# Kernel tuning notes

Measured on AMD Instinct MI355X. Metric: run time of the kernel, lower is better.

The kernel has to match this reference:

```python
import jax, jax.numpy as jnp
import numpy as np

C = 512
NUM_HEADS = 8
RF = 4          # reduction_factor
GROUPS = 8      # min(8, C//8)
EPS = 1e-5


def _pos_enc(h, w, c):
    # matches torch _create_positional_encoding; c must be divisible by 4
    y = jnp.arange(h, dtype=jnp.float32)[:, None] * jnp.ones((1, w), jnp.float32)
    x = jnp.ones((h, 1), jnp.float32) * jnp.arange(w, dtype=jnp.float32)[None, :]
    div = jnp.exp(jnp.arange(0, c // 2, 2, dtype=jnp.float32) * (-np.log(10000.0) / (c // 2)))  # [c//4]
    d = div[:, None, None]
    sy, cy = jnp.sin(y[None] * d), jnp.cos(y[None] * d)   # [c//4,h,w]
    sx, cx = jnp.sin(x[None] * d), jnp.cos(x[None] * d)
    pe = jnp.stack([sy, cy, sx, cx], axis=1).reshape(c, h, w)  # interleaved 0::4..3::4
    return pe[None] * 0.01


def _group_norm(x, w, b):
    B, Cc, H, W = x.shape
    g = x.reshape(B, GROUPS, -1)
    m = g.mean(-1, keepdims=True)
    v = g.var(-1, keepdims=True)
    g = (g - m) / jnp.sqrt(v + EPS)
    return g.reshape(B, Cc, H, W) * w[None, :, None, None] + b[None, :, None, None]


def setup_inputs() -> dict:
    key = jax.random.key(0)
    ks = jax.random.split(key, 4)
    B, H, W = 1, 256, 256
    x = jax.random.normal(ks[0], (B, C, H, W), jnp.float32)
    qkv_w = jax.random.normal(ks[1], (3 * C, C), jnp.float32) * 0.02
    proj_w = jax.random.normal(ks[2], (C, C), jnp.float32) * 0.02
    gamma = jax.random.normal(ks[3], (1,), jnp.float32)
    return {
        "x": x,
        "gn_weight": jnp.ones((C,), jnp.float32),
        "gn_bias": jnp.zeros((C,), jnp.float32),
        "qkv_w": qkv_w,
        "proj_w": proj_w,
        "proj_b": jnp.zeros((C,), jnp.float32),
        "gamma": gamma,
        "temperature": jnp.ones((NUM_HEADS, 1, 1), jnp.float32),
    }


def reference(x, gn_weight, gn_bias, qkv_w, proj_w, proj_b, gamma, temperature):
    B, Cc, H, W = x.shape
    hd = Cc // NUM_HEADS
    identity = x
    xn = _group_norm(x, gn_weight, gn_bias)
    # spatial reduction (AvgPool2d k=4 s=4); H,W > 32 in this config
    Hr, Wr = H // RF, W // RF
    xr = xn.reshape(B, Cc, Hr, RF, Wr, RF).mean(axis=(3, 5))
    xr = xr + _pos_enc(Hr, Wr, Cc)
    qkv = jnp.einsum('oc,bchw->bohw', qkv_w, xr)  # 1x1 conv, no bias
    q, k, v = jnp.split(qkv, 3, axis=1)
    N = Hr * Wr
    q = q.reshape(B, NUM_HEADS, hd, N) * (hd ** -0.5) * temperature[None]
    k = k.reshape(B, NUM_HEADS, hd, N)
    v = v.reshape(B, NUM_HEADS, hd, N)
    # chunked attention in torch == plain softmax attention (chunking over queries)
    attn = jax.nn.softmax(jnp.einsum('bhdn,bhdm->bhnm', q, k), axis=-1)
    out = jnp.einsum('bhnm,bhdm->bhdn', attn, v).reshape(B, Cc, Hr, Wr)
    out = jax.image.resize(out, (B, Cc, H, W), method='bilinear')  # align_corners=False
    out = jnp.einsum('oc,bchw->bohw', proj_w, out) + proj_b[None, :, None, None]
    # dropout in eval mode is identity
    return identity + gamma * out
```

## Files before the change

### kernel.cpp

```cpp
#include <hip/hip_runtime.h>
#include <hip/hip_bf16.h>


typedef __attribute__((ext_vector_type(4))) short short4v;
typedef __attribute__((ext_vector_type(8))) short short8v;
typedef __attribute__((ext_vector_type(4))) float f32x4;
typedef __attribute__((ext_vector_type(4))) unsigned int u32x4;

#define MFMA16(a, b, c) __builtin_amdgcn_mfma_f32_16x16x32_bf16(a, b, c, 0, 0, 0)

__device__ __forceinline__ unsigned short bf16r(float f) {
    unsigned int u = __builtin_bit_cast(unsigned int, f);
    u += 0x7fffu + ((u >> 16) & 1u);
    return (unsigned short)(u >> 16);
}
__device__ __forceinline__ float bff(unsigned short s) {
    unsigned int u = ((unsigned int)s) << 16;
    return __builtin_bit_cast(float, u);
}
__device__ __forceinline__ unsigned int fbits(float f) {
    return __builtin_bit_cast(unsigned int, f);
}

__global__ __launch_bounds__(256) void k_wconv(const float* __restrict__ qkv_w,
                                               const float* __restrict__ proj_w,
                                               const float* __restrict__ temp,
                                               unsigned short* __restrict__ wq_b,
                                               unsigned short* __restrict__ wp_b) {
    int idx = blockIdx.x * 256 + threadIdx.x;
    const int NQ = 1536 * 512;
    if (idx < NQ) {
        int o = idx >> 9;
        float sc = (o < 512) ? temp[o >> 6] * 0.125f : 1.0f;
        wq_b[idx] = bf16r(qkv_w[idx] * sc);
    } else {
        int j = idx - NQ;
        wp_b[j] = bf16r(proj_w[j]);
    }
}

__global__ __launch_bounds__(256) void k_pool(const float* __restrict__ x,
                                              float* __restrict__ xp,
                                              float* __restrict__ partials) {
    int hr = blockIdx.x;
    int c  = blockIdx.y;
    int t = threadIdx.x;
    int r = t >> 6, wq = t & 63;
    const float4* src = (const float4*)(x + (size_t)c * 65536 + (size_t)(4 * hr + r) * 256 + 4 * wq);
    float4 v = *src;
    float s4 = v.x + v.y + v.z + v.w;
    float q4 = v.x * v.x + v.y * v.y + v.z * v.z + v.w * v.w;

    __shared__ float sm[256];
    __shared__ float wq4[4];
    sm[t] = s4;
    float qq = q4;
#pragma unroll
    for (int off = 1; off < 64; off <<= 1) qq += __shfl_xor(qq, off, 64);
    if ((t & 63) == 0) wq4[t >> 6] = qq;
    __syncthreads();
    if (t < 64) {
        float cs = sm[t] + sm[64 + t] + sm[128 + t] + sm[192 + t];
        xp[(size_t)c * 4096 + hr * 64 + t] = cs * (1.0f / 16.0f);
        float ts = cs;
#pragma unroll
        for (int off = 1; off < 64; off <<= 1) ts += __shfl_xor(ts, off, 64);
        if (t == 0) {
            int g = c >> 6;
            int slot = (c & 63) * 64 + hr;
            partials[(size_t)(g * 4096 + slot) * 2 + 0] = ts;
            partials[(size_t)(g * 4096 + slot) * 2 + 1] = wq4[0] + wq4[1] + wq4[2] + wq4[3];
        }
    }
}

__global__ __launch_bounds__(256) void k_stats(const float* __restrict__ partials,
                                               float* __restrict__ gstats) {
    int g = blockIdx.x;
    int t = threadIdx.x;
    float s = 0.f, q = 0.f;
    for (int i = t; i < 4096; i += 256) {
        s += partials[(size_t)(g * 4096 + i) * 2 + 0];
        q += partials[(size_t)(g * 4096 + i) * 2 + 1];
    }
#pragma unroll
    for (int off = 1; off < 64; off <<= 1) {
        s += __shfl_xor(s, off, 64);
        q += __shfl_xor(q, off, 64);
    }
    __shared__ float ss[4], qs[4];
    if ((t & 63) == 0) { ss[t >> 6] = s; qs[t >> 6] = q; }
    __syncthreads();
    if (t == 0) {
        float S = ss[0] + ss[1] + ss[2] + ss[3];
        float Q = qs[0] + qs[1] + qs[2] + qs[3];
        const float inv = 1.0f / 4194304.0f;
        float m = S * inv;
        float var = Q * inv - m * m;
        gstats[2 * g] = m;
        gstats[2 * g + 1] = rsqrtf(var + 1e-5f);
    }
}

__global__ __launch_bounds__(256) void k_xr(const float* __restrict__ xp,
                                            const float* __restrict__ gs,
                                            const float* __restrict__ gw,
                                            const float* __restrict__ gb,
                                            unsigned short* __restrict__ xr) {
    int idx = blockIdx.x * 256 + threadIdx.x;
    int c = idx >> 12, n = idx & 4095;
    int hr = n >> 6, wr = n & 63;
    int g = c >> 6;
    float m = gs[2 * g], rs = gs[2 * g + 1];
    float xn = (xp[idx] - m) * rs * gw[c] + gb[c];
    int i = c >> 2, kind = c & 3;
    float di = expf(-(float)i * 0.07195578415606394f);
    float arg = ((kind < 2) ? (float)hr : (float)wr) * di;
    float pe = 0.01f * ((kind & 1) ? cosf(arg) : sinf(arg));
    xr[idx] = bf16r(xn + pe);
}

__global__ __launch_bounds__(256) void k_gemm(const unsigned short* __restrict__ A,
                                              const unsigned short* __restrict__ B,
                                              unsigned short* __restrict__ C) {
    __shared__ unsigned short As[128][36];
    __shared__ unsigned short Bs[128][36];
    int t = threadIdx.x;
    int w = t >> 6, l = t & 63, l15 = l & 15, lg = l >> 4;
    int wrow = w >> 1, wcol = w & 1;
    int m0 = blockIdx.y * 128, n0 = blockIdx.x * 128;
    f32x4 acc[4][4] = {};

    for (int k0 = 0; k0 < 512; k0 += 32) {
#pragma unroll
        for (int i = 0; i < 4; i++) {
            int idx = t + 256 * i;
            int row = idx >> 3, kc = idx & 7;
            short4v av = *(const short4v*)(A + (size_t)(m0 + row) * 512 + k0 + 4 * kc);
            *(short4v*)&As[row][4 * kc] = av;
        }
#pragma unroll
        for (int i = 0; i < 4; i++) {
            int idx = t + 256 * i;
            int kr = idx >> 5, nc = idx & 31;
            short4v bv = *(const short4v*)(B + (size_t)(k0 + kr) * 4096 + n0 + 4 * nc);
#pragma unroll
            for (int j = 0; j < 4; j++) Bs[4 * nc + j][kr] = (unsigned short)bv[j];
        }
        __syncthreads();

        short8v af[4];
#pragma unroll
        for (int mi = 0; mi < 4; mi++) {
            int ar = wrow * 64 + mi * 16 + l15;
            short4v a0 = *(const short4v*)&As[ar][4 * lg];
            short4v a1 = *(const short4v*)&As[ar][16 + 4 * lg];
            af[mi] = __builtin_shufflevector(a0, a1, 0, 1, 2, 3, 4, 5, 6, 7);
        }
#pragma unroll
        for (int ni = 0; ni < 4; ni++) {
            int bc = wcol * 64 + ni * 16 + l15;
            short4v b0 = *(const short4v*)&Bs[bc][4 * lg];
            short4v b1 = *(const short4v*)&Bs[bc][16 + 4 * lg];
            short8v bf = __builtin_shufflevector(b0, b1, 0, 1, 2, 3, 4, 5, 6, 7);
#pragma unroll
            for (int mi = 0; mi < 4; mi++) acc[mi][ni] = MFMA16(af[mi], bf, acc[mi][ni]);
        }
        __syncthreads();
    }
#pragma unroll
    for (int mi = 0; mi < 4; mi++)
#pragma unroll
        for (int ni = 0; ni < 4; ni++) {
            int row = m0 + wrow * 64 + mi * 16 + 4 * lg;
            int col = n0 + wcol * 64 + ni * 16 + l15;
#pragma unroll
            for (int r = 0; r < 4; r++)
                C[(size_t)(row + r) * 4096 + col] = bf16r(acc[mi][ni][r]);
        }
}

__global__ __launch_bounds__(256) void k_perm(const unsigned short* __restrict__ qkv,
                                              unsigned short* __restrict__ qtg,
                                              unsigned short* __restrict__ ktg,
                                              unsigned short* __restrict__ vtg) {
    __shared__ unsigned short lt[64][40];
    int t = threadIdx.x;
    int tile = blockIdx.x, h = blockIdx.y, z = blockIdx.z;
    int base = (z == 0 ? 0 : (z == 1 ? 512 : 1024)) + h * 64;
    int r = t >> 2, c4 = (t & 3) * 8;
    *(short8v*)&lt[r][c4] = *(const short8v*)(qkv + (size_t)(base + r) * 4096 + tile * 32 + c4);
    __syncthreads();
    unsigned short o[8];
    if (z < 2) {
        int col = t & 31, lgc = (t >> 5) & 3, s = t >> 7;
#pragma unroll
        for (int j = 0; j < 4; j++) {
            o[j] = lt[s * 32 + 4 * lgc + j][col];
            o[4 + j] = lt[s * 32 + 16 + 4 * lgc + j][col];
        }
    } else {
        int d = t & 63, lgc = t >> 6;
#pragma unroll
        for (int j = 0; j < 4; j++) {
            o[j] = lt[d][4 * lgc + j];
            o[4 + j] = lt[d][16 + 4 * lgc + j];
        }
    }
    unsigned short* dst = (z == 0 ? qtg : (z == 1 ? ktg : vtg)) + ((size_t)h * 128 + tile) * 2048 + t * 8;
    *(short8v*)dst = *(const short8v*)o;
}

__global__ __launch_bounds__(128) void k_attn(const unsigned short* __restrict__ qtg,
                                              const unsigned short* __restrict__ ktg,
                                              const unsigned short* __restrict__ vtg,
                                              unsigned short* __restrict__ opart,
                                              float* __restrict__ mlg) {
    int t = threadIdx.x;
    int l = t & 63, l15 = l & 15, lg = l >> 4, mw = t >> 6;
    int nu = blockIdx.x * 2 + mw, h = blockIdx.y, seg = blockIdx.z;

    const unsigned short* qb = qtg + ((size_t)h * 128 + nu) * 2048;
    const unsigned short* kb = ktg + ((size_t)h * 128 + seg * 32) * 2048;
    const unsigned short* vb = vtg + ((size_t)h * 128 + seg * 32) * 2048;

    short8v qf[2][2];
#pragma unroll
    for (int ng = 0; ng < 2; ng++)
#pragma unroll
        for (int s = 0; s < 2; s++)
            qf[ng][s] = *(const short8v*)(qb + s * 1024 + lg * 256 + ng * 128 + l15 * 8);

    f32x4 od[2][4] = {};
    float mrun[2] = {0.f, 0.f};
    float lrun[2] = {0.f, 0.f};
    const float LOG2E = 1.44269504f;

    auto loadK = [&](short8v (&kf)[2][2], int kt) {
#pragma unroll
        for (int mf = 0; mf < 2; mf++)
#pragma unroll
            for (int s = 0; s < 2; s++)
                kf[mf][s] = *(const short8v*)(kb + kt * 2048 + s * 1024 + lg * 256 + mf * 128 + l15 * 8);
    };
    auto loadV = [&](short8v (&vf)[4], int kt) {
#pragma unroll
        for (int dg = 0; dg < 4; dg++)
            vf[dg] = *(const short8v*)(vb + kt * 2048 + lg * 512 + dg * 128 + l15 * 8);
    };
    auto compute = [&](const short8v (&kf)[2][2], const short8v (&vf)[4]) {
#pragma unroll
        for (int ng = 0; ng < 2; ng++) {
            f32x4 s0 = {}, s1 = {};
            __builtin_amdgcn_s_setprio(1);
            s0 = MFMA16(kf[0][0], qf[ng][0], s0);
            s0 = MFMA16(kf[0][1], qf[ng][1], s0);
            s1 = MFMA16(kf[1][0], qf[ng][0], s1);
            s1 = MFMA16(kf[1][1], qf[ng][1], s1);
            __builtin_amdgcn_s_setprio(0);
            float pm = fmaxf(fmaxf(fmaxf(s0[0], s0[1]), fmaxf(s0[2], s0[3])),
                             fmaxf(fmaxf(s1[0], s1[1]), fmaxf(s1[2], s1[3])));
            pm = fmaxf(pm, __shfl_xor(pm, 16, 64));
            pm = fmaxf(pm, __shfl_xor(pm, 32, 64));
            if (!__all(pm <= mrun[ng] + 8.f)) {
                float mnew = fmaxf(mrun[ng], pm);
                float alpha = __expf(mrun[ng] - mnew);
#pragma unroll
                for (int dg = 0; dg < 4; dg++)
#pragma unroll
                    for (int r = 0; r < 4; r++) od[ng][dg][r] *= alpha;
                lrun[ng] *= alpha;
                mrun[ng] = mnew;
            }
            float mc = mrun[ng] * LOG2E;
            float p0[4], p1[4];
            float ps = 0.f;
#pragma unroll
            for (int r = 0; r < 4; r++) {
                p0[r] = __builtin_amdgcn_exp2f(fmaf(s0[r], LOG2E, -mc));
                p1[r] = __builtin_amdgcn_exp2f(fmaf(s1[r], LOG2E, -mc));
                ps += p0[r] + p1[r];
            }
            ps += __shfl_xor(ps, 16, 64);
            ps += __shfl_xor(ps, 32, 64);
            lrun[ng] += ps;
            u32x4 P;
            P[0] = __builtin_amdgcn_perm(fbits(p0[1]), fbits(p0[0]), 0x07060302u);
            P[1] = __builtin_amdgcn_perm(fbits(p0[3]), fbits(p0[2]), 0x07060302u);
            P[2] = __builtin_amdgcn_perm(fbits(p1[1]), fbits(p1[0]), 0x07060302u);
            P[3] = __builtin_amdgcn_perm(fbits(p1[3]), fbits(p1[2]), 0x07060302u);
            short8v pb = __builtin_bit_cast(short8v, P);
            __builtin_amdgcn_s_setprio(1);
#pragma unroll
            for (int dg = 0; dg < 4; dg++) od[ng][dg] = MFMA16(vf[dg], pb, od[ng][dg]);
            __builtin_amdgcn_s_setprio(0);
        }
    };

    short8v kfA[2][2], kfB[2][2], vfA[4], vfB[4];
    loadK(kfA, 0);
#pragma unroll 1
    for (int kt = 0; kt < 32; kt += 2) {
        loadV(vfA, kt);
        loadK(kfB, kt + 1);
        compute(kfA, vfA);
        loadV(vfB, kt + 1);
        if (kt + 2 < 32) loadK(kfA, kt + 2);
        compute(kfB, vfB);
    }

    unsigned short* op = opart + ((size_t)(seg * 512 + h * 64)) * 4096 + nu * 32;
#pragma unroll
    for (int ng = 0; ng < 2; ng++)
#pragma unroll
        for (int dg = 0; dg < 4; dg++)
#pragma unroll
            for (int r = 0; r < 4; r++) {
                int d = dg * 16 + 4 * lg + r;
                op[(size_t)d * 4096 + ng * 16 + l15] = bf16r(od[ng][dg][r]);
            }
    if (lg == 0) {
#pragma unroll
        for (int ng = 0; ng < 2; ng++) {
            float* mo = mlg + ((size_t)(seg * 8 + h) * 4096 + nu * 32 + ng * 16 + l15) * 2;
            mo[0] = mrun[ng];
            mo[1] = lrun[ng];
        }
    }
}

__global__ __launch_bounds__(256) void k_merge(const unsigned short* __restrict__ opart,
                                               const float* __restrict__ mlg,
                                               unsigned short* __restrict__ attn_b) {
    int bid = blockIdx.x, t = threadIdx.x;
    int row = bid >> 2;
    int n0 = (bid & 3) * 1024 + t * 4;
    int h = row >> 6;

    float m[4][4], lv[4][4];
#pragma unroll
    for (int s = 0; s < 4; s++) {
        const float2* mlp = (const float2*)(mlg + ((size_t)(s * 8 + h) * 4096 + n0) * 2);
#pragma unroll
        for (int j = 0; j < 4; j++) {
            float2 v = mlp[j];
            m[s][j] = v.x;
            lv[s][j] = v.y;
        }
    }
    short4v ov[4];
#pragma unroll
    for (int s = 0; s < 4; s++)
        ov[s] = *(const short4v*)(opart + (size_t)s * 2097152 + (size_t)row * 4096 + n0);

    unsigned short res[4];
#pragma unroll
    for (int j = 0; j < 4; j++) {
        float M = fmaxf(fmaxf(m[0][j], m[1][j]), fmaxf(m[2][j], m[3][j]));
        float den = 0.f, num = 0.f;
#pragma unroll
        for (int s = 0; s < 4; s++) {
            float wgt = __expf(m[s][j] - M);
            den += wgt * lv[s][j];
            num += wgt * bff((unsigned short)ov[s][j]);
        }
        res[j] = bf16r(num / den);
    }
    *(short4v*)(attn_b + (size_t)row * 4096 + n0) = *(const short4v*)res;
}

__global__ __launch_bounds__(256) void k_up(const float* __restrict__ x,
                                            const unsigned short* __restrict__ low,
                                            const float* __restrict__ proj_b,
                                            const float* __restrict__ gamma,
                                            float* __restrict__ out) {
    int t = threadIdx.x;
    int hs = t >> 6;
    int hh = blockIdx.x * 4 + hs;
    int c = blockIdx.y;
    int a = t & 63;

    int ph = hh & 3, Ah = hh >> 2;
    int y0 = Ah + ((ph < 2) ? -1 : 0);
    float fy = (ph < 2) ? (0.625f + 0.25f * ph) : (0.125f + 0.25f * (ph - 2));
    int y1 = min(y0 + 1, 63); y0 = max(y0, 0);

    const unsigned short* L0 = low + (size_t)c * 4096 + y0 * 64;
    const unsigned short* L1 = low + (size_t)c * 4096 + y1 * 64;
    int am = max(a - 1, 0), ap = min(a + 1, 63);
    float gy = 1.f - fy;
    float vm = gy * bff(L0[am]) + fy * bff(L1[am]);
    float v0 = gy * bff(L0[a])  + fy * bff(L1[a]);
    float vp = gy * bff(L0[ap]) + fy * bff(L1[ap]);

    float pb = proj_b[c], g = gamma[0];
    size_t idx = (size_t)c * 65536 + (size_t)hh * 256 + a * 4;
    float4 xi = *(const float4*)(x + idx);
    float4 o;
    o.x = xi.x + g * (0.375f * vm + 0.625f * v0 + pb);
    o.y = xi.y + g * (0.125f * vm + 0.875f * v0 + pb);
    o.z = xi.z + g * (0.875f * v0 + 0.125f * vp + pb);
    o.w = xi.w + g * (0.625f * v0 + 0.375f * vp + pb);
    *(float4*)(out + idx) = o;
}

extern "C" void kernel_launch(void* const* d_in, const int* in_sizes, int n_in,
                              void* d_out, int out_size, void* d_ws, size_t ws_size,
                              hipStream_t stream) {
    const float* x     = (const float*)d_in[0];
    const float* gnw   = (const float*)d_in[1];
    const float* gnb   = (const float*)d_in[2];
    const float* qkvw  = (const float*)d_in[3];
    const float* projw = (const float*)d_in[4];
    const float* projb = (const float*)d_in[5];
    const float* gamma = (const float*)d_in[6];
    const float* temp  = (const float*)d_in[7];

    char* ws = (char*)d_ws;
    const size_t MB = 1u << 20;
    float* gstats          = (float*)(ws + 0);
    float* partials        = (float*)(ws + 1024);
    float* xp              = (float*)(ws + 1 * MB);
    unsigned short* qtg    = (unsigned short*)(ws + 1 * MB);
    unsigned short* ktg    = (unsigned short*)(ws + 5 * MB);
    unsigned short* xr_b   = (unsigned short*)(ws + 9 * MB);
    unsigned short* vtg    = (unsigned short*)(ws + 9 * MB);
    unsigned short* wq_b   = (unsigned short*)(ws + 13 * MB);
    unsigned short* wp_b   = (unsigned short*)(ws + 15 * MB);
    unsigned short* qkv_b  = (unsigned short*)(ws + 16 * MB);
    unsigned short* attn_b = (unsigned short*)(ws + 28 * MB);
    unsigned short* low_b  = (unsigned short*)(ws + 32 * MB);
    float* out = (float*)d_out;
    unsigned short* opart = (unsigned short*)d_out;
    float* mlg = (float*)((char*)d_out + 16 * MB);

    k_wconv<<<4096, 256, 0, stream>>>(qkvw, projw, temp, wq_b, wp_b);
    k_pool<<<dim3(64, 512), 256, 0, stream>>>(x, xp, partials);
    k_stats<<<8, 256, 0, stream>>>(partials, gstats);
    k_xr<<<8192, 256, 0, stream>>>(xp, gstats, gnw, gnb, xr_b);
    k_gemm<<<dim3(32, 12), 256, 0, stream>>>(wq_b, xr_b, qkv_b);
    k_perm<<<dim3(128, 8, 3), 256, 0, stream>>>(qkv_b, qtg, ktg, vtg);
    k_attn<<<dim3(64, 8, 4), 128, 0, stream>>>(qtg, ktg, vtg, opart, mlg);
    k_merge<<<2048, 256, 0, stream>>>(opart, mlg, attn_b);
    k_gemm<<<dim3(32, 4), 256, 0, stream>>>(wp_b, attn_b, low_b);
    k_up<<<dim3(64, 512), 256, 0, stream>>>(x, low_b, projb, gamma, out);
}
```

Measured before the change: 209.2 us.

## Share K/V tiles via LDS across 8 waves and split keys into 8 segments

The attention kernel now runs 8 waves per block, and all of them share K/V tiles staged into double-buffered LDS with async global_load_lds, where before each wave loaded its own K/V straight from global memory. The key range is split into 8 segments instead of 4, which changes the grid shape, the merge kernel's segment count and the mlg offset. The aim is to cut redundant global/L2 traffic for K/V and keep parallelism up. The cost is two barriers per iteration, more partial outputs to merge, and a larger scratch footprint in the output buffer.

```diff
diff --git a/kernel.cpp b/kernel.cpp
--- a/kernel.cpp
+++ b/kernel.cpp
@@ -20,6 +20,12 @@
 }
 __device__ __forceinline__ unsigned int fbits(float f) {
     return __builtin_bit_cast(unsigned int, f);
+}
+
+typedef const __attribute__((address_space(1))) unsigned int guint;
+typedef __attribute__((address_space(3))) unsigned int luint;
+__device__ __forceinline__ void gload16(const void* g, void* l) {
+    __builtin_amdgcn_global_load_lds((guint*)g, (luint*)l, 16, 0, 0);
 }
 
 __global__ __launch_bounds__(256) void k_wconv(const float* __restrict__ qkv_w,
@@ -211,18 +217,21 @@
     *(short8v*)dst = *(const short8v*)o;
 }
 
-__global__ __launch_bounds__(128) void k_attn(const unsigned short* __restrict__ qtg,
+__global__ __launch_bounds__(512) void k_attn(const unsigned short* __restrict__ qtg,
                                               const unsigned short* __restrict__ ktg,
                                               const unsigned short* __restrict__ vtg,
                                               unsigned short* __restrict__ opart,
                                               float* __restrict__ mlg) {
-    int t = threadIdx.x;
-    int l = t & 63, l15 = l & 15, lg = l >> 4, mw = t >> 6;
-    int nu = blockIdx.x * 2 + mw, h = blockIdx.y, seg = blockIdx.z;
+    __shared__ __align__(16) unsigned short kbuf[2][2048];
+    __shared__ __align__(16) unsigned short vbuf[2][2048];
+    int t = threadIdx.x;
+    int l = t & 63, l15 = l & 15, lg = l >> 4, w = t >> 6;
+    int qt = blockIdx.x, h = blockIdx.y, seg = blockIdx.z;
+    int nu = qt * 8 + w;
 
     const unsigned short* qb = qtg + ((size_t)h * 128 + nu) * 2048;
-    const unsigned short* kb = ktg + ((size_t)h * 128 + seg * 32) * 2048;
-    const unsigned short* vb = vtg + ((size_t)h * 128 + seg * 32) * 2048;
+    const unsigned short* kb = ktg + ((size_t)h * 128 + seg * 16) * 2048;
+    const unsigned short* vb = vtg + ((size_t)h * 128 + seg * 16) * 2048;
 
     short8v qf[2][2];
 #pragma unroll
@@ -230,25 +239,44 @@
 #pragma unroll
         for (int s = 0; s < 2; s++)
             qf[ng][s] = *(const short8v*)(qb + s * 1024 + lg * 256 + ng * 128 + l15 * 8);
+
+    int st = t & 255;
+    const unsigned short* sp = ((t >= 256) ? vb : kb) + st * 8;
+    unsigned short* ldst = ((t >= 256) ? &vbuf[0][0] : &kbuf[0][0]) + st * 8;
 
     f32x4 od[2][4] = {};
     float mrun[2] = {0.f, 0.f};
     float lrun[2] = {0.f, 0.f};
     const float LOG2E = 1.44269504f;
 
-    auto loadK = [&](short8v (&kf)[2][2], int kt) {
+#define STAGE(kt, u) gload16(sp + (kt) * 2048, ldst + (u) * 2048)
+
+    STAGE(0, 0);
+
+    int u = 0;
+#pragma unroll 1
+    for (int kt = 0; kt < 16; kt++) {
+        if (kt < 15) {
+            STAGE(kt + 1, u ^ 1);
+            asm volatile("s_waitcnt vmcnt(1)" ::: "memory");
+        } else {
+            asm volatile("s_waitcnt vmcnt(0)" ::: "memory");
+        }
+        __builtin_amdgcn_s_barrier();
+
+        const unsigned short* kl = &kbuf[u][0];
+        const unsigned short* vl = &vbuf[u][0];
+
+        short8v kf[2][2], vf[4];
 #pragma unroll
         for (int mf = 0; mf < 2; mf++)
 #pragma unroll
             for (int s = 0; s < 2; s++)
-                kf[mf][s] = *(const short8v*)(kb + kt * 2048 + s * 1024 + lg * 256 + mf * 128 + l15 * 8);
-    };
-    auto loadV = [&](short8v (&vf)[4], int kt) {
+                kf[mf][s] = *(const short8v*)(kl + s * 1024 + lg * 256 + mf * 128 + l15 * 8);
 #pragma unroll
         for (int dg = 0; dg < 4; dg++)
-            vf[dg] = *(const short8v*)(vb + kt * 2048 + lg * 512 + dg * 128 + l15 * 8);
-    };
-    auto compute = [&](const short8v (&kf)[2][2], const short8v (&vf)[4]) {
+            vf[dg] = *(const short8v*)(vl + lg * 512 + dg * 128 + l15 * 8);
+
 #pragma unroll
         for (int ng = 0; ng < 2; ng++) {
             f32x4 s0 = {}, s1 = {};
@@ -295,19 +323,11 @@
             for (int dg = 0; dg < 4; dg++) od[ng][dg] = MFMA16(vf[dg], pb, od[ng][dg]);
             __builtin_amdgcn_s_setprio(0);
         }
-    };
-
-    short8v kfA[2][2], kfB[2][2], vfA[4], vfB[4];
-    loadK(kfA, 0);
-#pragma unroll 1
-    for (int kt = 0; kt < 32; kt += 2) {
-        loadV(vfA, kt);
-        loadK(kfB, kt + 1);
-        compute(kfA, vfA);
-        loadV(vfB, kt + 1);
-        if (kt + 2 < 32) loadK(kfA, kt + 2);
-        compute(kfB, vfB);
-    }
+
+        __builtin_amdgcn_s_barrier();
+        u ^= 1;
+    }
+#undef STAGE
 
     unsigned short* op = opart + ((size_t)(seg * 512 + h * 64)) * 4096 + nu * 32;
 #pragma unroll
@@ -337,9 +357,9 @@
     int n0 = (bid & 3) * 1024 + t * 4;
     int h = row >> 6;
 
-    float m[4][4], lv[4][4];
-#pragma unroll
-    for (int s = 0; s < 4; s++) {
+    float m[8][4], lv[8][4];
+#pragma unroll
+    for (int s = 0; s < 8; s++) {
         const float2* mlp = (const float2*)(mlg + ((size_t)(s * 8 + h) * 4096 + n0) * 2);
 #pragma unroll
         for (int j = 0; j < 4; j++) {
@@ -348,18 +368,20 @@
             lv[s][j] = v.y;
         }
     }
-    short4v ov[4];
-#pragma unroll
-    for (int s = 0; s < 4; s++)
+    short4v ov[8];
+#pragma unroll
+    for (int s = 0; s < 8; s++)
         ov[s] = *(const short4v*)(opart + (size_t)s * 2097152 + (size_t)row * 4096 + n0);
 
     unsigned short res[4];
 #pragma unroll
     for (int j = 0; j < 4; j++) {
-        float M = fmaxf(fmaxf(m[0][j], m[1][j]), fmaxf(m[2][j], m[3][j]));
+        float M = m[0][j];
+#pragma unroll
+        for (int s = 1; s < 8; s++) M = fmaxf(M, m[s][j]);
         float den = 0.f, num = 0.f;
 #pragma unroll
-        for (int s = 0; s < 4; s++) {
+        for (int s = 0; s < 8; s++) {
             float wgt = __expf(m[s][j] - M);
             den += wgt * lv[s][j];
             num += wgt * bff((unsigned short)ov[s][j]);
@@ -432,7 +454,7 @@
     unsigned short* low_b  = (unsigned short*)(ws + 32 * MB);
     float* out = (float*)d_out;
     unsigned short* opart = (unsigned short*)d_out;
-    float* mlg = (float*)((char*)d_out + 16 * MB);
+    float* mlg = (float*)((char*)d_out + 32 * MB);
 
     k_wconv<<<4096, 256, 0, stream>>>(qkvw, projw, temp, wq_b, wp_b);
     k_pool<<<dim3(64, 512), 256, 0, stream>>>(x, xp, partials);
@@ -440,7 +462,7 @@
     k_xr<<<8192, 256, 0, stream>>>(xp, gstats, gnw, gnb, xr_b);
     k_gemm<<<dim3(32, 12), 256, 0, stream>>>(wq_b, xr_b, qkv_b);
     k_perm<<<dim3(128, 8, 3), 256, 0, stream>>>(qkv_b, qtg, ktg, vtg);
-    k_attn<<<dim3(64, 8, 4), 128, 0, stream>>>(qtg, ktg, vtg, opart, mlg);
+    k_attn<<<dim3(16, 8, 8), 512, 0, stream>>>(qtg, ktg, vtg, opart, mlg);
     k_merge<<<2048, 256, 0, stream>>>(opart, mlg, attn_b);
     k_gemm<<<dim3(32, 4), 256, 0, stream>>>(wp_b, attn_b, low_b);
     k_up<<<dim3(64, 512), 256, 0, stream>>>(x, low_b, projb, gamma, out);
```

Result: no change. 205.2 us (-1.9%).
